# Kernel tuning notes

Measured on AMD Instinct MI355X. Metric: run time of the kernel, lower is better.

Reference implementation:

```python
import jax, jax.numpy as jnp
from jax import lax
from jax.scipy.special import logsumexp
import numpy as np

IMSIZE = 256
DS = 2
EPS = 0.1          # geomloss: eps = blur**p = (reg**0.5)**2 = reg
RHO = 1.0          # geomloss: rho = reach**p = (reg_m**0.5)**2 = reg_m
ALPHA = 0.8
CONF_DELAY = 400.0
CONF_ITER = 0.0    # buffer starts at 0; incremented after forward
N_ITER = 50        # fixed-eps Sinkhorn sweeps (geomloss uses eps-scaling to the same fixed point)
B, M = 4, 256
G = IMSIZE // DS   # 128
N = G * G          # 16384 grid cells


def make_grid():
    coords = jnp.linspace(0.5 / G, 1.0 - 0.5 / G, G)
    Yg, Xg = jnp.meshgrid(coords, coords, indexing='xy')  # torch: Y, X = meshgrid(c, c, indexing='xy')
    return jnp.stack([Xg, Yg], axis=-1).reshape(-1, 2)


def sq_cost(x, y):
    # 0.5 * ||x - y||^2, shape (N, M)
    d2 = jnp.sum(x * x, -1)[:, None] + jnp.sum(y * y, -1)[None, :] - 2.0 * (x @ y.T)
    return 0.5 * jnp.maximum(d2, 0.0)


def sinkhorn_potentials(log_a, log_b, C):
    # Unbalanced log-domain Sinkhorn with KL marginal relaxation (damping tau).
    tau = RHO / (RHO + EPS)
    la, lb, Cd = map(lax.stop_gradient, (log_a, log_b, C))
    def body(_, fg):
        f, g = fg
        f = -tau * EPS * logsumexp(lb[None, :] + (g[None, :] - Cd) / EPS, axis=1)
        g = -tau * EPS * logsumexp(la[:, None] + (f[:, None] - Cd) / EPS, axis=0)
        return (f, g)
    f0 = jnp.zeros(log_a.shape, log_a.dtype)
    g0 = jnp.zeros(log_b.shape, log_b.dtype)
    f, g = lax.fori_loop(0, N_ITER, body, (f0, g0))
    # final symmetric extrapolation carries gradients (geomloss last_extrapolation / envelope theorem)
    f_new = -tau * EPS * logsumexp(log_b[None, :] + (g[None, :] - C) / EPS, axis=1)
    g_new = -tau * EPS * logsumexp(log_a[:, None] + (f[:, None] - C) / EPS, axis=0)
    return f_new, g_new


def uot_cost(a, log_a, b, log_b, C):
    f, g = sinkhorn_potentials(log_a, log_b, C)
    w = RHO + EPS / 2.0   # geomloss UnbalancedWeight forward scaling
    return w * (jnp.sum(a * (1.0 - jnp.exp(-f / RHO))) + jnp.sum(b * (1.0 - jnp.exp(-g / RHO))))


def per_sample(dens, pts, grid):
    a = jnp.clip(dens.reshape(-1), 1e-8)          # (N,)
    y = pts / IMSIZE                               # (M, 2) in [0,1]^2
    b = jnp.ones((pts.shape[0],), dens.dtype)      # (M,)
    C = sq_cost(grid, y)                           # (N, M)
    # --- recompute_beta (torch.no_grad) ---
    la = jnp.log(lax.stop_gradient(a))
    lb = jnp.log(b)
    Cd = lax.stop_gradient(C)
    F, Gp = sinkhorn_potentials(la, lb, Cd)
    log_pi = (F[:, None] + Gp[None, :] - Cd) / EPS + la[:, None] + lb[None, :]
    residual = jnp.exp(log_pi).sum(0) - b
    lamb = ALPHA * jax.nn.sigmoid(10.0 * (CONF_ITER / CONF_DELAY - 0.5))
    new_b = lax.stop_gradient(jnp.clip(b + lamb * residual, 1e-8))
    # --- loss_fn(a, grid, new_b, y) ---
    return uot_cost(a, jnp.log(a), new_b, jnp.log(new_b), C)


def setup_inputs() -> dict:
    key = jax.random.key(0)
    k1, k2 = jax.random.split(key)
    unnormed_density = jax.random.uniform(k1, (B, 1, G, G), jnp.float32)
    points = jax.random.uniform(k2, (B, M, 2), jnp.float32) * IMSIZE
    return {"unnormed_density": unnormed_density, "points": points, "grid": make_grid()}


def reference(unnormed_density, points, grid):
    losses = jax.vmap(lambda d, p: per_sample(d, p, grid))(unnormed_density[:, 0], points)
    return jnp.sum(losses)
```

## Files before the change

### kernel.cpp

```cpp
#include <hip/hip_runtime.h>


typedef __attribute__((ext_vector_type(4))) float f32x4;
typedef __attribute__((ext_vector_type(8))) short short8;

#define TAU_F     0.9090909090909091f
#define TEPS_F    0.09090909090909091f
#define LAMB_F    0.005354280739427885f
#define NEG5L2E  -7.213475204444817f

static __device__ __forceinline__ float hexp2(float x) {
  float r; asm("v_exp_f32 %0, %1" : "=v"(r) : "v"(x)); return r;
}
static __device__ __forceinline__ float hlog2(float x) {
  float r; asm("v_log_f32 %0, %1" : "=v"(r) : "v"(x)); return r;
}
static __device__ __forceinline__ float powm(float x, float p) {
  return hexp2(p * hlog2(x));
}
static __device__ __forceinline__ float pklo(unsigned u) {
  union { unsigned i; float f; } v; v.i = u << 16; return v.f;
}
static __device__ __forceinline__ float pkhi(unsigned u) {
  union { unsigned i; float f; } v; v.i = u & 0xffff0000u; return v.f;
}
static __device__ __forceinline__ unsigned cvtpk(float lo, float hi) {
  unsigned r;
  asm("v_cvt_pk_bf16_f32 %0, %1, %2" : "=v"(r) : "v"(lo), "v"(hi));
  return r;
}
static __device__ __forceinline__ f32x4 mfma16(uint4 a, uint4 b, f32x4 c) {
  return __builtin_amdgcn_mfma_f32_16x16x32_bf16(
      __builtin_bit_cast(short8, a), __builtin_bit_cast(short8, b), c, 0, 0, 0);
}

__global__ void __launch_bounds__(512, 2)
uot_kernel(const float* __restrict__ dens, const float* __restrict__ pts,
           float* __restrict__ out, unsigned long long* __restrict__ ws) {
  __shared__ float ymx[256], ymy[256], psi[256], nb[256], tb[256], tps[256];
  __shared__ float tp[2][256];
  __shared__ float red[8];
  __shared__ uint4 Vl4[320];
  unsigned short* Vl = (unsigned short*)Vl4;

  const int s = blockIdx.x >> 3, b = blockIdx.x & 7;
  const int ib = b >> 2, jb = b & 3;
  const int i0 = ib * 64, j0 = jb * 32;
  const int t = threadIdx.x, l = t & 63, w = t >> 6;
  const int wi = w >> 1, wj = w & 1;
  const int ii = w >> 2, mi = w & 3;
  const int lr = l & 15, lq = l >> 4;

  unsigned long long* tpair = ws + (size_t)s * 4096;
  const float* dp = dens + s * 16384;
  const float* pp = pts + s * 512;

  if (t < 256) {
    ymx[t] = pp[2 * t] * (1.f / 256.f);
    ymy[t] = pp[2 * t + 1] * (1.f / 256.f);
    psi[t] = 1.f;
    nb[t]  = 1.f;
  }
  __syncthreads();

  uint4 A_f[8], B_f[8], B_g[4];
  uint2 A_t[2][4];
  float a_f[4];
  {
    float gxa = (i0 + wi * 16 + lr + 0.5f) * (1.f / 128.f);
    float gya = (j0 + wj * 16 + lr + 0.5f) * (1.f / 128.f);
    #pragma unroll
    for (int ks = 0; ks < 8; ++ks) {
      unsigned qa[4], qb[4];
      #pragma unroll
      for (int e4 = 0; e4 < 4; ++e4) {
        int m0 = ks * 32 + 8 * lq + 2 * e4;
        float dx0 = gxa - ymx[m0], dx1 = gxa - ymx[m0 + 1];
        float dy0 = gya - ymy[m0], dy1 = gya - ymy[m0 + 1];
        qa[e4] = cvtpk(hexp2(dx0 * dx0 * NEG5L2E), hexp2(dx1 * dx1 * NEG5L2E));
        qb[e4] = cvtpk(hexp2(dy0 * dy0 * NEG5L2E), hexp2(dy1 * dy1 * NEG5L2E));
      }
      A_f[ks] = make_uint4(qa[0], qa[1], qa[2], qa[3]);
      B_f[ks] = make_uint4(qb[0], qb[1], qb[2], qb[3]);
    }
    #pragma unroll
    for (int mt = 0; mt < 4; ++mt) {
      float ym = ymy[mi * 64 + mt * 16 + lr];
      unsigned q[4];
      #pragma unroll
      for (int e4 = 0; e4 < 4; ++e4) {
        float g0 = (j0 + 8 * lq + 2 * e4 + 0.5f) * (1.f / 128.f);
        float d0 = g0 - ym, d1 = d0 + (1.f / 128.f);
        q[e4] = cvtpk(hexp2(d0 * d0 * NEG5L2E), hexp2(d1 * d1 * NEG5L2E));
      }
      B_g[mt] = make_uint4(q[0], q[1], q[2], q[3]);
    }
    #pragma unroll
    for (int it = 0; it < 2; ++it)
      #pragma unroll
      for (int mt = 0; mt < 4; ++mt) {
        float ym = ymx[mi * 64 + mt * 16 + lr];
        float g0 = (i0 + ii * 32 + it * 16 + 4 * lq + 0.5f) * (1.f / 128.f);
        float d0 = g0 - ym, d1 = d0 + (1.f / 128.f);
        float d2 = d0 + (2.f / 128.f), d3 = d0 + (3.f / 128.f);
        A_t[it][mt].x = cvtpk(hexp2(d0 * d0 * NEG5L2E), hexp2(d1 * d1 * NEG5L2E));
        A_t[it][mt].y = cvtpk(hexp2(d2 * d2 * NEG5L2E), hexp2(d3 * d3 * NEG5L2E));
      }
    #pragma unroll
    for (int e = 0; e < 4; ++e)
      a_f[e] = fmaxf(dp[(i0 + wi * 16 + 4 * lq + e) * 128 + (j0 + wj * 16 + lr)],
                     1e-8f);
  }

  f32x4 fA;
  unsigned mygen = 0;
  int par = 0;

  auto f_update = [&]() {
    f32x4 acc = {0.f, 0.f, 0.f, 0.f};
    #pragma unroll
    for (int ks = 0; ks < 8; ++ks) {
      int mb = ks * 32 + 8 * lq;
      float4 p0 = *(const float4*)(psi + mb);
      float4 p1 = *(const float4*)(psi + mb + 4);
      const unsigned* ar = (const unsigned*)&A_f[ks];
      uint4 wf;
      wf.x = cvtpk(pklo(ar[0]) * p0.x, pkhi(ar[0]) * p0.y);
      wf.y = cvtpk(pklo(ar[1]) * p0.z, pkhi(ar[1]) * p0.w);
      wf.z = cvtpk(pklo(ar[2]) * p1.x, pkhi(ar[2]) * p1.y);
      wf.w = cvtpk(pklo(ar[3]) * p1.z, pkhi(ar[3]) * p1.w);
      acc = mfma16(wf, B_f[ks], acc);
    }
    fA = acc;
  };

  auto g_update = [&](int mode) {
    #pragma unroll
    for (int e = 0; e < 4; ++e) {
      float phi = powm(fA[e], -TAU_F);
      int il = wi * 16 + 4 * lq + e;
      int jl = wj * 16 + lr;
      union { float f; unsigned i; } v; v.f = a_f[e] * phi;
      unsigned bi = v.i + 0x7fffu + ((v.i >> 16) & 1u);
      Vl[il * 40 + jl] = (unsigned short)(bi >> 16);
    }
    __syncthreads();
    uint4 vfr[2];
    #pragma unroll
    for (int it = 0; it < 2; ++it)
      vfr[it] = *(const uint4*)(Vl + (ii * 32 + it * 16 + lr) * 40 + 8 * lq);
    f32x4 gA[2][4];
    #pragma unroll
    for (int it = 0; it < 2; ++it)
      #pragma unroll
      for (int mt = 0; mt < 4; ++mt) {
        f32x4 z = {0.f, 0.f, 0.f, 0.f};
        gA[it][mt] = mfma16(vfr[it], B_g[mt], z);
      }
    #pragma unroll
    for (int mt = 0; mt < 4; ++mt) {
      float acc = 0.f;
      #pragma unroll
      for (int it = 0; it < 2; ++it) {
        uint2 u = A_t[it][mt];
        acc += pklo(u.x) * gA[it][mt][0];
        acc += pkhi(u.x) * gA[it][mt][1];
        acc += pklo(u.y) * gA[it][mt][2];
        acc += pkhi(u.y) * gA[it][mt][3];
      }
      acc += __shfl_xor(acc, 16);
      acc += __shfl_xor(acc, 32);
      if (l < 16) tp[ii][mi * 64 + mt * 16 + lr] = acc;
    }
    __syncthreads();
    const unsigned target = mygen + 1;
    if (t < 256) {
      float own = tp[0][t] + tp[1][t];
      union { float f; unsigned i; } ov; ov.f = own;
      unsigned long long pu = ((unsigned long long)target << 32) | ov.i;
      __hip_atomic_store(&tpair[par * 2048 + b * 256 + t], pu,
                         __ATOMIC_RELAXED, __HIP_MEMORY_SCOPE_AGENT);
      float tm;
      bool ok;
      do {
        ok = true; tm = 0.f;
        #pragma unroll
        for (int k = 0; k < 8; ++k) {
          unsigned long long p =
              __hip_atomic_load(&tpair[par * 2048 + k * 256 + t],
                                __ATOMIC_RELAXED, __HIP_MEMORY_SCOPE_AGENT);
          ok &= ((unsigned)(p >> 32) >= target);
          union { unsigned i; float f; } pv; pv.i = (unsigned)p;
          tm += pv.f;
        }
        if (!ok) __builtin_amdgcn_s_sleep(1);
      } while (!ok);
      if (mode == 2) {
        float r   = psi[t] * tm - 1.f;
        float nbv = fmaxf(1.f + LAMB_F * r, 1e-8f);
        nb[t] = nbv;
        psi[t] = nbv;
      } else {
        float ps = powm(tm, -TAU_F);
        psi[t] = (mode == 1 ? nb[t] : 1.f) * ps;
        tb[t] = tm;
      }
    }
    mygen++;
    par ^= 1;
    __syncthreads();
  };

  #pragma unroll 1
  for (int phase = 0; phase < 2; ++phase) {
    #pragma unroll 1
    for (int iter = 0; iter < 51; ++iter) {
      f_update();
      if (iter < 50) g_update(phase);
    }
    if (phase == 0) g_update(2);
  }

  float ls = 0.f;
  #pragma unroll
  for (int e = 0; e < 4; ++e)
    ls += a_f[e] * (1.f - powm(fA[e], TEPS_F));
  #pragma unroll
  for (int off = 32; off >= 1; off >>= 1) ls += __shfl_xor(ls, off);
  if (l == 0) red[w] = ls;
  __syncthreads();
  if (t < 256) tps[t] = nb[t] * (1.f - powm(tb[t], TEPS_F));
  __syncthreads();
  if (t < 64) {
    float v = (b == 0) ? (tps[t] + tps[t + 64] + tps[t + 128] + tps[t + 192])
                       : 0.f;
    #pragma unroll
    for (int off = 32; off >= 1; off >>= 1) v += __shfl_xor(v, off);
    if (t == 0) {
      float la = 0.f;
      #pragma unroll
      for (int k = 0; k < 8; ++k) la += red[k];
      atomicAdd(out, 1.05f * (la + v));
    }
  }
}

extern "C" void kernel_launch(void* const* d_in, const int* in_sizes, int n_in,
                              void* d_out, int out_size, void* d_ws, size_t ws_size,
                              hipStream_t stream) {
  const float* dens = (const float*)d_in[0];
  const float* pts  = (const float*)d_in[1];
  float* out = (float*)d_out;
  if (ws_size < 131072) return;
  (void)hipMemsetAsync(d_out, 0, (size_t)out_size * sizeof(float), stream);
  (void)hipMemsetAsync(d_ws, 0, 131072, stream);
  hipLaunchKernelGGL(uot_kernel, dim3(32), dim3(512), 0, stream,
                     dens, pts, out, (unsigned long long*)d_ws);
}
```

Measured before the change: 265.7 us.

## Split each sample across sixteen 256-thread blocks instead of eight 512-thread blocks

Repartitions the grid so each sample is handled by 16 blocks of 4 waves, each owning a 32x32 tile, instead of 8 blocks of 8 waves with 64x32 tiles. Each wave now covers a full 64-point slice for the transpose pass, so the intra-block cross-wave partial sum and the second LDS buffer go away. This spreads work over more CUs and shortens per-block critical paths. The cost is twice as many participants in the global spin barrier every iteration, more atomic loads per poll, and a larger workspace.

```diff
diff --git a/kernel.cpp b/kernel.cpp
--- a/kernel.cpp
+++ b/kernel.cpp
@@ -34,24 +34,23 @@
       __builtin_bit_cast(short8, a), __builtin_bit_cast(short8, b), c, 0, 0, 0);
 }
 
-__global__ void __launch_bounds__(512, 2)
+__global__ void __launch_bounds__(256)
 uot_kernel(const float* __restrict__ dens, const float* __restrict__ pts,
            float* __restrict__ out, unsigned long long* __restrict__ ws) {
   __shared__ float ymx[256], ymy[256], psi[256], nb[256], tb[256], tps[256];
-  __shared__ float tp[2][256];
-  __shared__ float red[8];
-  __shared__ uint4 Vl4[320];
+  __shared__ float tp[256];
+  __shared__ float red[4];
+  __shared__ uint4 Vl4[160];
   unsigned short* Vl = (unsigned short*)Vl4;
 
-  const int s = blockIdx.x >> 3, b = blockIdx.x & 7;
-  const int ib = b >> 2, jb = b & 3;
-  const int i0 = ib * 64, j0 = jb * 32;
+  const int s = blockIdx.x >> 4, blk = blockIdx.x & 15;
+  const int bi = blk >> 2, bj = blk & 3;
+  const int i0 = bi * 32, j0 = bj * 32;
   const int t = threadIdx.x, l = t & 63, w = t >> 6;
   const int wi = w >> 1, wj = w & 1;
-  const int ii = w >> 2, mi = w & 3;
   const int lr = l & 15, lq = l >> 4;
 
-  unsigned long long* tpair = ws + (size_t)s * 4096;
+  unsigned long long* tpair = ws + (size_t)s * 8192;
   const float* dp = dens + s * 16384;
   const float* pp = pts + s * 512;
 
@@ -85,7 +84,7 @@
     }
     #pragma unroll
     for (int mt = 0; mt < 4; ++mt) {
-      float ym = ymy[mi * 64 + mt * 16 + lr];
+      float ym = ymy[w * 64 + mt * 16 + lr];
       unsigned q[4];
       #pragma unroll
       for (int e4 = 0; e4 < 4; ++e4) {
@@ -99,8 +98,8 @@
     for (int it = 0; it < 2; ++it)
       #pragma unroll
       for (int mt = 0; mt < 4; ++mt) {
-        float ym = ymx[mi * 64 + mt * 16 + lr];
-        float g0 = (i0 + ii * 32 + it * 16 + 4 * lq + 0.5f) * (1.f / 128.f);
+        float ym = ymx[w * 64 + mt * 16 + lr];
+        float g0 = (i0 + it * 16 + 4 * lq + 0.5f) * (1.f / 128.f);
         float d0 = g0 - ym, d1 = d0 + (1.f / 128.f);
         float d2 = d0 + (2.f / 128.f), d3 = d0 + (3.f / 128.f);
         A_t[it][mt].x = cvtpk(hexp2(d0 * d0 * NEG5L2E), hexp2(d1 * d1 * NEG5L2E));
@@ -141,14 +140,14 @@
       int il = wi * 16 + 4 * lq + e;
       int jl = wj * 16 + lr;
       union { float f; unsigned i; } v; v.f = a_f[e] * phi;
-      unsigned bi = v.i + 0x7fffu + ((v.i >> 16) & 1u);
-      Vl[il * 40 + jl] = (unsigned short)(bi >> 16);
+      unsigned bi16 = v.i + 0x7fffu + ((v.i >> 16) & 1u);
+      Vl[il * 40 + jl] = (unsigned short)(bi16 >> 16);
     }
     __syncthreads();
     uint4 vfr[2];
     #pragma unroll
     for (int it = 0; it < 2; ++it)
-      vfr[it] = *(const uint4*)(Vl + (ii * 32 + it * 16 + lr) * 40 + 8 * lq);
+      vfr[it] = *(const uint4*)(Vl + (it * 16 + lr) * 40 + 8 * lq);
     f32x4 gA[2][4];
     #pragma unroll
     for (int it = 0; it < 2; ++it)
@@ -170,24 +169,24 @@
       }
       acc += __shfl_xor(acc, 16);
       acc += __shfl_xor(acc, 32);
-      if (l < 16) tp[ii][mi * 64 + mt * 16 + lr] = acc;
+      if (l < 16) tp[w * 64 + mt * 16 + lr] = acc;
     }
     __syncthreads();
     const unsigned target = mygen + 1;
-    if (t < 256) {
-      float own = tp[0][t] + tp[1][t];
+    {
+      float own = tp[t];
       union { float f; unsigned i; } ov; ov.f = own;
       unsigned long long pu = ((unsigned long long)target << 32) | ov.i;
-      __hip_atomic_store(&tpair[par * 2048 + b * 256 + t], pu,
+      __hip_atomic_store(&tpair[par * 4096 + blk * 256 + t], pu,
                          __ATOMIC_RELAXED, __HIP_MEMORY_SCOPE_AGENT);
       float tm;
       bool ok;
       do {
         ok = true; tm = 0.f;
         #pragma unroll
-        for (int k = 0; k < 8; ++k) {
+        for (int k = 0; k < 16; ++k) {
           unsigned long long p =
-              __hip_atomic_load(&tpair[par * 2048 + k * 256 + t],
+              __hip_atomic_load(&tpair[par * 4096 + k * 256 + t],
                                 __ATOMIC_RELAXED, __HIP_MEMORY_SCOPE_AGENT);
           ok &= ((unsigned)(p >> 32) >= target);
           union { unsigned i; float f; } pv; pv.i = (unsigned)p;
@@ -232,14 +231,12 @@
   if (t < 256) tps[t] = nb[t] * (1.f - powm(tb[t], TEPS_F));
   __syncthreads();
   if (t < 64) {
-    float v = (b == 0) ? (tps[t] + tps[t + 64] + tps[t + 128] + tps[t + 192])
-                       : 0.f;
+    float v = (blk == 0) ? (tps[t] + tps[t + 64] + tps[t + 128] + tps[t + 192])
+                         : 0.f;
     #pragma unroll
     for (int off = 32; off >= 1; off >>= 1) v += __shfl_xor(v, off);
     if (t == 0) {
-      float la = 0.f;
-      #pragma unroll
-      for (int k = 0; k < 8; ++k) la += red[k];
+      float la = red[0] + red[1] + red[2] + red[3];
       atomicAdd(out, 1.05f * (la + v));
     }
   }
@@ -251,9 +248,9 @@
   const float* dens = (const float*)d_in[0];
   const float* pts  = (const float*)d_in[1];
   float* out = (float*)d_out;
-  if (ws_size < 131072) return;
+  if (ws_size < 262144) return;
   (void)hipMemsetAsync(d_out, 0, (size_t)out_size * sizeof(float), stream);
-  (void)hipMemsetAsync(d_ws, 0, 131072, stream);
-  hipLaunchKernelGGL(uot_kernel, dim3(32), dim3(512), 0, stream,
+  (void)hipMemsetAsync(d_ws, 0, 262144, stream);
+  hipLaunchKernelGGL(uot_kernel, dim3(64), dim3(256), 0, stream,
                      dens, pts, out, (unsigned long long*)d_ws);
 }
```

After: 287.6 us. 1.08x slower.

## Add transposed sc0 fast-path exchange and remap blocks to colocate sample groups

Applied to the files above, without the earlier changes.

Each block now also writes its partial column sums into a transposed layout with sc0 stores, so a thread can poll all eight peers' values for its column using four vector loads per spin instead of eight separate atomic loads. If peers don't arrive within a bounded spin count, it falls back to the original atomic path. The grid is doubled and the block index mapping swapped, so the eight blocks of one sample get strided block IDs (likely landing on the same XCD/L2), and half the blocks exit immediately. This relies on sc0 visibility semantics across blocks and doubles the workspace.

```diff
diff --git a/kernel.cpp b/kernel.cpp
--- a/kernel.cpp
+++ b/kernel.cpp
@@ -8,6 +8,7 @@
 #define TEPS_F    0.09090909090909091f
 #define LAMB_F    0.005354280739427885f
 #define NEG5L2E  -7.213475204444817f
+#define FAST_SPINS 128
 
 static __device__ __forceinline__ float hexp2(float x) {
   float r; asm("v_exp_f32 %0, %1" : "=v"(r) : "v"(x)); return r;
@@ -32,6 +33,11 @@
 static __device__ __forceinline__ f32x4 mfma16(uint4 a, uint4 b, f32x4 c) {
   return __builtin_amdgcn_mfma_f32_16x16x32_bf16(
       __builtin_bit_cast(short8, a), __builtin_bit_cast(short8, b), c, 0, 0, 0);
+}
+static __device__ __forceinline__ void st_sc0(unsigned long long* p,
+                                              unsigned long long v) {
+  asm volatile("global_store_dwordx2 %0, %1, off sc0"
+               :: "v"(p), "v"(v) : "memory");
 }
 
 __global__ void __launch_bounds__(512, 2)
@@ -43,7 +49,8 @@
   __shared__ uint4 Vl4[320];
   unsigned short* Vl = (unsigned short*)Vl4;
 
-  const int s = blockIdx.x >> 3, b = blockIdx.x & 7;
+  const int s = blockIdx.x & 7, b = blockIdx.x >> 3;
+  if (s >= 4) return;
   const int ib = b >> 2, jb = b & 3;
   const int i0 = ib * 64, j0 = jb * 32;
   const int t = threadIdx.x, l = t & 63, w = t >> 6;
@@ -52,6 +59,7 @@
   const int lr = l & 15, lq = l >> 4;
 
   unsigned long long* tpair = ws + (size_t)s * 4096;
+  unsigned long long* tfast = ws + 16384 + (size_t)s * 4096;
   const float* dp = dens + s * 16384;
   const float* pp = pts + s * 512;
 
@@ -115,6 +123,7 @@
   f32x4 fA;
   unsigned mygen = 0;
   int par = 0;
+  bool use_fast = true;
 
   auto f_update = [&]() {
     f32x4 acc = {0.f, 0.f, 0.f, 0.f};
@@ -178,23 +187,56 @@
       float own = tp[0][t] + tp[1][t];
       union { float f; unsigned i; } ov; ov.f = own;
       unsigned long long pu = ((unsigned long long)target << 32) | ov.i;
+      st_sc0(&tfast[par * 2048 + t * 8 + b], pu);
       __hip_atomic_store(&tpair[par * 2048 + b * 256 + t], pu,
                          __ATOMIC_RELAXED, __HIP_MEMORY_SCOPE_AGENT);
-      float tm;
-      bool ok;
-      do {
-        ok = true; tm = 0.f;
-        #pragma unroll
-        for (int k = 0; k < 8; ++k) {
-          unsigned long long p =
-              __hip_atomic_load(&tpair[par * 2048 + k * 256 + t],
-                                __ATOMIC_RELAXED, __HIP_MEMORY_SCOPE_AGENT);
-          ok &= ((unsigned)(p >> 32) >= target);
-          union { unsigned i; float f; } pv; pv.i = (unsigned)p;
-          tm += pv.f;
+      float tm = 0.f;
+      bool got = false;
+      if (use_fast) {
+        unsigned long long* fbase = &tfast[par * 2048 + t * 8];
+        #pragma unroll 1
+        for (int spin = 0; spin < FAST_SPINS; ++spin) {
+          uint4 q0, q1, q2, q3;
+          asm volatile(
+            "global_load_dwordx4 %0, %4, off sc0\n\t"
+            "global_load_dwordx4 %1, %4, off offset:16 sc0\n\t"
+            "global_load_dwordx4 %2, %4, off offset:32 sc0\n\t"
+            "global_load_dwordx4 %3, %4, off offset:48 sc0\n\t"
+            "s_waitcnt vmcnt(0)"
+            : "=&v"(q0), "=&v"(q1), "=&v"(q2), "=&v"(q3)
+            : "v"(fbase) : "memory");
+          if (q0.y >= target && q0.w >= target && q1.y >= target &&
+              q1.w >= target && q2.y >= target && q2.w >= target &&
+              q3.y >= target && q3.w >= target) {
+            union { unsigned i; float f; } v0, v1, v2, v3, v4, v5, v6, v7;
+            v0.i = q0.x; v1.i = q0.z; v2.i = q1.x; v3.i = q1.z;
+            v4.i = q2.x; v5.i = q2.z; v6.i = q3.x; v7.i = q3.z;
+            tm = ((((((v0.f + v1.f) + v2.f) + v3.f) + v4.f) + v5.f) + v6.f)
+                 + v7.f;
+            got = true;
+            break;
+          }
+          __builtin_amdgcn_s_sleep(1);
         }
-        if (!ok) __builtin_amdgcn_s_sleep(1);
-      } while (!ok);
+        if (!got) use_fast = false;
+      }
+      if (!got) {
+        bool ok;
+        do {
+          ok = true; float ts = 0.f;
+          #pragma unroll
+          for (int k = 0; k < 8; ++k) {
+            unsigned long long p =
+                __hip_atomic_load(&tpair[par * 2048 + k * 256 + t],
+                                  __ATOMIC_RELAXED, __HIP_MEMORY_SCOPE_AGENT);
+            ok &= ((unsigned)(p >> 32) >= target);
+            union { unsigned i; float f; } pv; pv.i = (unsigned)p;
+            ts += pv.f;
+          }
+          if (ok) tm = ts;
+          else __builtin_amdgcn_s_sleep(1);
+        } while (!ok);
+      }
       if (mode == 2) {
         float r   = psi[t] * tm - 1.f;
         float nbv = fmaxf(1.f + LAMB_F * r, 1e-8f);
@@ -251,9 +293,9 @@
   const float* dens = (const float*)d_in[0];
   const float* pts  = (const float*)d_in[1];
   float* out = (float*)d_out;
-  if (ws_size < 131072) return;
+  if (ws_size < 262144) return;
   (void)hipMemsetAsync(d_out, 0, (size_t)out_size * sizeof(float), stream);
-  (void)hipMemsetAsync(d_ws, 0, 131072, stream);
-  hipLaunchKernelGGL(uot_kernel, dim3(32), dim3(512), 0, stream,
+  (void)hipMemsetAsync(d_ws, 0, 262144, stream);
+  hipLaunchKernelGGL(uot_kernel, dim3(64), dim3(512), 0, stream,
                      dens, pts, out, (unsigned long long*)d_ws);
 }
```

New measurement: 341.2 us. 1.28x slower.
